# Performance work log

Hardware: AMD Instinct MI355X
Metric: run time of the kernel (lower is better)

Reference implementation:

```python
import jax, jax.numpy as jnp
import numpy as np

N = 100000   # nodes
E = 1600000  # edges
F = 128      # num_features
NF = 4       # n_factor
D = 64       # n_dim = dim // n_factor = 256 // 4
NL = 3       # n_layer
G = 128      # num graphs in batch


def setup_inputs() -> dict:
    key = jax.random.key(0)
    ks = jax.random.split(key, 10)
    s = 0.05
    x = jax.random.normal(ks[0], (N, F), jnp.float32)
    edge_index = jax.random.randint(ks[1], (2, E), 0, N)
    att = jax.random.uniform(ks[2], (NF, E), jnp.float32)
    batch = jnp.sort(jax.random.randint(ks[3], (N,), 0, G))
    lin_W = jax.random.normal(ks[4], (NF, F, D), jnp.float32) * s
    lin_b = jnp.zeros((NF, D), jnp.float32)
    conv_Wrel = jax.random.normal(ks[5], (NF, NL, D, D), jnp.float32) * s
    conv_brel = jnp.zeros((NF, NL, D), jnp.float32)
    conv_Wroot = jax.random.normal(ks[6], (NF, NL, D, D), jnp.float32) * s
    gru_Wih = jax.random.normal(ks[7], (NF, 3 * D, D), jnp.float32) * s
    gru_Whh = jax.random.normal(ks[8], (NF, 3 * D, D), jnp.float32) * s
    gru_bih = jnp.zeros((NF, 3 * D), jnp.float32)
    gru_bhh = jnp.zeros((NF, 3 * D), jnp.float32)
    return dict(x=x, edge_index=edge_index, att=att, batch=batch,
                lin_W=lin_W, lin_b=lin_b,
                conv_Wrel=conv_Wrel, conv_brel=conv_brel, conv_Wroot=conv_Wroot,
                gru_Wih=gru_Wih, gru_Whh=gru_Whh, gru_bih=gru_bih, gru_bhh=gru_bhh,
                num_graphs=G)


def _gru_cell(xin, h, Wih, Whh, bih, bhh):
    # torch.nn.GRU single step: r,z,n gates
    gi = xin @ Wih.T + bih  # [N, 3D]
    gh = h @ Whh.T + bhh
    ir, iz, inn = jnp.split(gi, 3, axis=-1)
    hr, hz, hn = jnp.split(gh, 3, axis=-1)
    r = jax.nn.sigmoid(ir + hr)
    z = jax.nn.sigmoid(iz + hz)
    n = jnp.tanh(inn + r * hn)
    return (1.0 - z) * n + z * h


def reference(x, edge_index, att, batch, lin_W, lin_b, conv_Wrel, conv_brel,
              conv_Wroot, gru_Wih, gru_Whh, gru_bih, gru_bhh, num_graphs):
    src, dst = edge_index[0], edge_index[1]
    counts = jax.ops.segment_sum(jnp.ones((N,), x.dtype), batch, num_segments=num_graphs)
    counts = jnp.maximum(counts, 1.0)[:, None]
    outs, feats = [], []
    for f in range(NF):
        w = att[f][:, None]                       # [E,1] edge weights for this factor
        out = x @ lin_W[f] + lin_b[f]             # [N,D]
        h = out                                   # initial GRU hidden state
        for l in range(NL):
            # GraphConv: lin_rel(scatter_add(w * x_src -> dst)) + lin_root(x)
            agg = jax.ops.segment_sum(out[src] * w, dst, num_segments=N)
            m = jax.nn.relu(agg @ conv_Wrel[f, l] + conv_brel[f, l] + out @ conv_Wroot[f, l])
            h = _gru_cell(m, h, gru_Wih[f], gru_Whh[f], gru_bih[f], gru_bhh[f])
            out = h
        feats.append(out)
        # global mean pool
        outs.append(jax.ops.segment_sum(out, batch, num_segments=num_graphs) / counts)
    return (jnp.stack(outs), jnp.stack(feats))
```

## Files before the change

kernel.cpp:

```cpp
#include <hip/hip_runtime.h>

#define NN   100000
#define EE   1600000
#define FDIM 128
#define NFAC 4
#define DD   64
#define NLAY 3
#define GG   128
#define ROW  (NFAC * DD)

#define PF_STRIDE 57344
#define OFF_WREL  8192
#define OFF_WROOT 20480
#define OFF_WIH   32768
#define OFF_WHH   45056
#define PREP_TOTAL (NFAC * PF_STRIDE)

typedef __bf16 bf16x8_t __attribute__((ext_vector_type(8)));
typedef float  f32x4_t  __attribute__((ext_vector_type(4)));

__device__ __forceinline__ unsigned short f2bf(float x) {
    unsigned u = __float_as_uint(x);
    u += 0x7fffu + ((u >> 16) & 1u);
    return (unsigned short)(u >> 16);
}
__device__ __forceinline__ float b2f(unsigned short h) {
    return __uint_as_float(((unsigned)h) << 16);
}
__device__ __forceinline__ float sigm(float x) { return 1.f / (1.f + __expf(-x)); }
__device__ __forceinline__ float tanh_f(float x) {
    float t = __expf(-2.f * fabsf(x));
    float r = (1.f - t) / (1.f + t);
    return x >= 0.f ? r : -r;
}

__global__ __launch_bounds__(256) void k_init(int* deg, int* cursor, float* outs) {
    int i = blockIdx.x * 256 + threadIdx.x;
    if (i < NN) { deg[i] = 0; cursor[i] = 0; }
    if (i < NFAC * GG * DD) outs[i] = 0.f;
}

__global__ __launch_bounds__(256) void k_prep(const float* x, const float* linW,
                                              const float* wrel, const float* wroot,
                                              const float* wih, const float* whh,
                                              unsigned short* x16, unsigned short* prep) {
    for (int i = blockIdx.x * 256 + threadIdx.x; i < NN * FDIM; i += gridDim.x * 256)
        x16[i] = f2bf(x[i]);
    for (int idx = blockIdx.x * 256 + threadIdx.x; idx < PREP_TOTAL; idx += gridDim.x * 256) {
        int f = idx / PF_STRIDE, r = idx % PF_STRIDE;
        int e, KB, mode, l = 0;
        if (r < OFF_WREL)       { e = r;                 KB = 4; mode = 0; }
        else if (r < OFF_WROOT) { int rr = r - OFF_WREL;  l = rr >> 12; e = rr & 4095; KB = 2; mode = 1; }
        else if (r < OFF_WIH)   { int rr = r - OFF_WROOT; l = rr >> 12; e = rr & 4095; KB = 2; mode = 2; }
        else if (r < OFF_WHH)   { e = r - OFF_WIH;        KB = 2; mode = 3; }
        else                    { e = r - OFF_WHH;        KB = 2; mode = 4; }
        int j = e & 7, lane = (e >> 3) & 63, t = e >> 9;
        int kb = t % KB, nt = t / KB;
        int k = kb * 32 + (lane >> 4) * 8 + j;
        int n = nt * 16 + (lane & 15);
        float v;
        if (mode == 0)      v = linW[(f * FDIM + k) * DD + n];
        else if (mode == 1) v = wrel[((f * 3 + l) * DD + k) * DD + n];
        else if (mode == 2) v = wroot[((f * 3 + l) * DD + k) * DD + n];
        else if (mode == 3) v = wih[(f * 192 + n) * DD + k];
        else                v = whh[(f * 192 + n) * DD + k];
        prep[idx] = f2bf(v);
    }
}

__global__ __launch_bounds__(256) void k_count(const int* batch, float* counts) {
    __shared__ int lb[GG + 1];
    int t = threadIdx.x;
    if (t <= GG) {
        int lo = 0, hi = NN;
        while (lo < hi) { int mid = (lo + hi) >> 1; if (batch[mid] < t) lo = mid + 1; else hi = mid; }
        lb[t] = lo;
    }
    __syncthreads();
    if (t < GG) counts[t] = (float)(lb[t + 1] - lb[t]);
}

__global__ __launch_bounds__(256) void k_deg(const int* ei, int* deg) {
    int e = blockIdx.x * 256 + threadIdx.x;
    if (e < EE) atomicAdd(&deg[ei[EE + e]], 1);
}
__global__ __launch_bounds__(256) void k_scan1(const int* deg, int* row_pos, int* bsum) {
    __shared__ int lds[256];
    int tid = threadIdx.x, idx = blockIdx.x * 256 + tid;
    int v = (idx < NN) ? deg[idx] : 0;
    lds[tid] = v; __syncthreads();
    for (int s = 1; s < 256; s <<= 1) {
        int t = (tid >= s) ? lds[tid - s] : 0;
        __syncthreads();
        lds[tid] += t;
        __syncthreads();
    }
    if (idx < NN) row_pos[idx] = lds[tid] - v;
    if (tid == 255) bsum[blockIdx.x] = lds[255];
}
__global__ __launch_bounds__(512) void k_scan2(int* bsum) {
    __shared__ int lds[512];
    int tid = threadIdx.x;
    int v = (tid < 391) ? bsum[tid] : 0;
    lds[tid] = v; __syncthreads();
    for (int s = 1; s < 512; s <<= 1) {
        int t = (tid >= s) ? lds[tid - s] : 0;
        __syncthreads();
        lds[tid] += t;
        __syncthreads();
    }
    bsum[tid] = lds[tid] - v;
}
__global__ __launch_bounds__(256) void k_rowptr(const int* row_pos, const int* boff, int* row_ptr) {
    int i = blockIdx.x * 256 + threadIdx.x;
    if (i < NN) row_ptr[i] = row_pos[i] + boff[i >> 8];
    if (i == 0) row_ptr[NN] = EE;
}
__global__ __launch_bounds__(256) void k_fill(const int* ei, const float* att,
                                              const int* row_ptr, int* cursor,
                                              int* csr_src, float* csr_att) {
    int e = blockIdx.x * 256 + threadIdx.x;
    if (e >= EE) return;
    int d = ei[EE + e];
    int slot = row_ptr[d] + atomicAdd(&cursor[d], 1);
    csr_src[slot] = ei[e];
    *(float4*)(csr_att + (size_t)slot * 4) =
        make_float4(att[e], att[EE + e], att[2 * EE + e], att[3 * EE + e]);
}

__global__ __launch_bounds__(256) void k_lin(const unsigned short* x16, const unsigned short* prep,
                                             const float* linb, unsigned short* out16) {
    int n0 = blockIdx.x * 64;
    __shared__ unsigned short xs[64 * 136];
    int tid = threadIdx.x;
    for (int t = tid; t < 1024; t += 256) {
        int row = t >> 4, seg = t & 15;
        int gn = n0 + row; if (gn >= NN) gn = NN - 1;
        *(uint4*)(xs + row * 136 + seg * 8) = *(const uint4*)(x16 + (size_t)gn * FDIM + seg * 8);
    }
    __syncthreads();
    int w = tid >> 6, lane = tid & 63, mrow = lane & 15, q = lane >> 4;
    const unsigned short* wp = prep + w * PF_STRIDE;
    bf16x8_t a[4][4];
#pragma unroll
    for (int mt = 0; mt < 4; mt++)
#pragma unroll
        for (int kb = 0; kb < 4; kb++)
            a[mt][kb] = *(const bf16x8_t*)(xs + (mt * 16 + mrow) * 136 + kb * 32 + q * 8);
#pragma unroll
    for (int nt = 0; nt < 4; nt++) {
        bf16x8_t b[4];
#pragma unroll
        for (int kb = 0; kb < 4; kb++)
            b[kb] = *(const bf16x8_t*)(wp + ((nt * 4 + kb) * 64 + lane) * 8);
        int col = nt * 16 + mrow;
        float bias = linb[w * DD + col];
#pragma unroll
        for (int mt = 0; mt < 4; mt++) {
            f32x4_t acc = {0.f, 0.f, 0.f, 0.f};
#pragma unroll
            for (int kb = 0; kb < 4; kb++)
                acc = __builtin_amdgcn_mfma_f32_16x16x32_bf16(a[mt][kb], b[kb], acc, 0, 0, 0);
#pragma unroll
            for (int r = 0; r < 4; r++) {
                int node = n0 + mt * 16 + q * 4 + r;
                if (node < NN) out16[(size_t)node * ROW + w * DD + col] = f2bf(acc[r] + bias);
            }
        }
    }
}

__global__ __launch_bounds__(256) void k_gather(const int* row_ptr, const int* csr_src, const float* csr_att,
                                                const unsigned short* out16, unsigned short* agg16) {
    int wave = threadIdx.x >> 6, lane = threadIdx.x & 63;
    int n = blockIdx.x * 4 + wave;
    if (n >= NN) return;
    int row = row_ptr[n], end = row_ptr[n + 1];
    int total = end - row;
    int fsel = lane >> 4, loff = lane * 4;
    float a0 = 0.f, a1 = 0.f, a2 = 0.f, a3 = 0.f;
    for (int base = 0; base < total; base += 8) {
        int s[8]; float w[8];
#pragma unroll
        for (int j = 0; j < 8; j++) {
            int e = base + j;
            int idx = row + (e < total ? e : total - 1);
            s[j] = csr_src[idx];
            float ww = csr_att[(size_t)idx * 4 + fsel];
            w[j] = (e < total) ? ww : 0.f;
        }
        uint2 v[8];
#pragma unroll
        for (int j = 0; j < 8; j++)
            v[j] = *(const uint2*)(out16 + (size_t)s[j] * ROW + loff);
#pragma unroll
        for (int j = 0; j < 8; j++) {
            a0 = fmaf(w[j], __uint_as_float(v[j].x << 16), a0);
            a1 = fmaf(w[j], __uint_as_float(v[j].x & 0xffff0000u), a1);
            a2 = fmaf(w[j], __uint_as_float(v[j].y << 16), a2);
            a3 = fmaf(w[j], __uint_as_float(v[j].y & 0xffff0000u), a3);
        }
    }
    ushort4 r;
    r.x = f2bf(a0); r.y = f2bf(a1); r.z = f2bf(a2); r.w = f2bf(a3);
    *(ushort4*)(agg16 + (size_t)n * ROW + loff) = r;
}

__global__ __launch_bounds__(256) void k_layer(int l, const unsigned short* agg16, unsigned short* out16,
                                               const unsigned short* prep, const float* brel,
                                               const float* bih, const float* bhh,
                                               float* feats, int last) {
    int f = blockIdx.y, n0 = blockIdx.x * 64;
    __shared__ unsigned short A1[64 * 72];
    __shared__ unsigned short A2[64 * 72];
    __shared__ unsigned short Mt[64 * 72];
    int tid = threadIdx.x;
    for (int t = tid; t < 512; t += 256) {
        int row = t >> 3, seg = t & 7;
        int gn = n0 + row; if (gn >= NN) gn = NN - 1;
        *(uint4*)(A1 + row * 72 + seg * 8) = *(const uint4*)(agg16 + (size_t)gn * ROW + f * DD + seg * 8);
        *(uint4*)(A2 + row * 72 + seg * 8) = *(const uint4*)(out16 + (size_t)gn * ROW + f * DD + seg * 8);
    }
    __syncthreads();
    int w = tid >> 6, lane = tid & 63, mrow = lane & 15, q = lane >> 4;
    const unsigned short* wrel  = prep + f * PF_STRIDE + OFF_WREL  + l * 4096;
    const unsigned short* wroot = prep + f * PF_STRIDE + OFF_WROOT + l * 4096;

    {
        bf16x8_t wr1[2], wr2[2];
#pragma unroll
        for (int kb = 0; kb < 2; kb++) {
            wr1[kb] = *(const bf16x8_t*)(wrel  + ((w * 2 + kb) * 64 + lane) * 8);
            wr2[kb] = *(const bf16x8_t*)(wroot + ((w * 2 + kb) * 64 + lane) * 8);
        }
        int col = w * 16 + mrow;
        float bias = brel[(f * 3 + l) * DD + col];
#pragma unroll
        for (int mt = 0; mt < 4; mt++) {
            f32x4_t acc = {0.f, 0.f, 0.f, 0.f};
#pragma unroll
            for (int kb = 0; kb < 2; kb++) {
                bf16x8_t a1 = *(const bf16x8_t*)(A1 + (mt * 16 + mrow) * 72 + kb * 32 + q * 8);
                acc = __builtin_amdgcn_mfma_f32_16x16x32_bf16(a1, wr1[kb], acc, 0, 0, 0);
                bf16x8_t a2 = *(const bf16x8_t*)(A2 + (mt * 16 + mrow) * 72 + kb * 32 + q * 8);
                acc = __builtin_amdgcn_mfma_f32_16x16x32_bf16(a2, wr2[kb], acc, 0, 0, 0);
            }
#pragma unroll
            for (int r = 0; r < 4; r++) {
                float mv = acc[r] + bias;
                mv = mv > 0.f ? mv : 0.f;
                Mt[(mt * 16 + q * 4 + r) * 72 + col] = f2bf(mv);
            }
        }
    }
    __syncthreads();

    const unsigned short* wih = prep + f * PF_STRIDE + OFF_WIH;
    const unsigned short* whh = prep + f * PF_STRIDE + OFF_WHH;
    bf16x8_t Br[2], Bz[2], Bn[2], Cr[2], Cz[2], Cn[2];
#pragma unroll
    for (int kb = 0; kb < 2; kb++) {
        Br[kb] = *(const bf16x8_t*)(wih + (((w)     * 2 + kb) * 64 + lane) * 8);
        Bz[kb] = *(const bf16x8_t*)(wih + (((w + 4) * 2 + kb) * 64 + lane) * 8);
        Bn[kb] = *(const bf16x8_t*)(wih + (((w + 8) * 2 + kb) * 64 + lane) * 8);
        Cr[kb] = *(const bf16x8_t*)(whh + (((w)     * 2 + kb) * 64 + lane) * 8);
        Cz[kb] = *(const bf16x8_t*)(whh + (((w + 4) * 2 + kb) * 64 + lane) * 8);
        Cn[kb] = *(const bf16x8_t*)(whh + (((w + 8) * 2 + kb) * 64 + lane) * 8);
    }
    int col = w * 16 + mrow;
    float bi_r = bih[f * 192 + col],        bh_r = bhh[f * 192 + col];
    float bi_z = bih[f * 192 + 64 + col],   bh_z = bhh[f * 192 + 64 + col];
    float bi_n = bih[f * 192 + 128 + col],  bh_n = bhh[f * 192 + 128 + col];
#pragma unroll
    for (int mt = 0; mt < 4; mt++) {
        f32x4_t ir = {0.f,0.f,0.f,0.f}, iz = {0.f,0.f,0.f,0.f}, in_ = {0.f,0.f,0.f,0.f};
        f32x4_t hr = {0.f,0.f,0.f,0.f}, hz = {0.f,0.f,0.f,0.f}, hn  = {0.f,0.f,0.f,0.f};
#pragma unroll
        for (int kb = 0; kb < 2; kb++) {
            bf16x8_t am = *(const bf16x8_t*)(Mt + (mt * 16 + mrow) * 72 + kb * 32 + q * 8);
            bf16x8_t ah = *(const bf16x8_t*)(A2 + (mt * 16 + mrow) * 72 + kb * 32 + q * 8);
            ir  = __builtin_amdgcn_mfma_f32_16x16x32_bf16(am, Br[kb], ir, 0, 0, 0);
            iz  = __builtin_amdgcn_mfma_f32_16x16x32_bf16(am, Bz[kb], iz, 0, 0, 0);
            in_ = __builtin_amdgcn_mfma_f32_16x16x32_bf16(am, Bn[kb], in_, 0, 0, 0);
            hr  = __builtin_amdgcn_mfma_f32_16x16x32_bf16(ah, Cr[kb], hr, 0, 0, 0);
            hz  = __builtin_amdgcn_mfma_f32_16x16x32_bf16(ah, Cz[kb], hz, 0, 0, 0);
            hn  = __builtin_amdgcn_mfma_f32_16x16x32_bf16(ah, Cn[kb], hn, 0, 0, 0);
        }
#pragma unroll
        for (int r = 0; r < 4; r++) {
            float rg = sigm(ir[r] + bi_r + hr[r] + bh_r);
            float z  = sigm(iz[r] + bi_z + hz[r] + bh_z);
            float nn = tanh_f(in_[r] + bi_n + rg * (hn[r] + bh_n));
            float h  = b2f(A2[(mt * 16 + q * 4 + r) * 72 + col]);
            float hp = (1.f - z) * nn + z * h;
            int node = n0 + mt * 16 + q * 4 + r;
            if (node < NN) {
                out16[(size_t)node * ROW + f * DD + col] = f2bf(hp);
                if (last) feats[((size_t)f * NN + node) * DD + col] = hp;
            }
        }
    }
}

__global__ __launch_bounds__(256) void k_pool(const float* feats, const int* batch, float* outs) {
    int f = blockIdx.y, w = threadIdx.x >> 6, lane = threadIdx.x & 63;
    int nbase = blockIdx.x * 256 + w * 64;
    if (nbase >= NN) return;
    int g_cur = batch[nbase];
    float acc = 0.f;
    for (int i = 0; i < 64; i++) {
        int n = nbase + i;
        if (n >= NN) break;
        int g = batch[n];
        float v = feats[((size_t)f * NN + n) * DD + lane];
        if (g != g_cur) {
            atomicAdd(&outs[(f * GG + g_cur) * DD + lane], acc);
            acc = v; g_cur = g;
        } else acc += v;
    }
    atomicAdd(&outs[(f * GG + g_cur) * DD + lane], acc);
}
__global__ __launch_bounds__(256) void k_norm(float* outs, const float* counts) {
    int i = blockIdx.x * 256 + threadIdx.x;
    if (i < NFAC * GG * DD) {
        int g = (i >> 6) & (GG - 1);
        outs[i] /= fmaxf(counts[g], 1.f);
    }
}

extern "C" void kernel_launch(void* const* d_in, const int* in_sizes, int n_in,
                              void* d_out, int out_size, void* d_ws, size_t ws_size,
                              hipStream_t stream) {
    const float* x    = (const float*)d_in[0];
    const int*   ei   = (const int*)d_in[1];
    const float* att  = (const float*)d_in[2];
    const int*   batch= (const int*)d_in[3];
    const float* linW = (const float*)d_in[4];
    const float* linb = (const float*)d_in[5];
    const float* wrel = (const float*)d_in[6];
    const float* brel = (const float*)d_in[7];
    const float* wroot= (const float*)d_in[8];
    const float* wih  = (const float*)d_in[9];
    const float* whh  = (const float*)d_in[10];
    const float* bih  = (const float*)d_in[11];
    const float* bhh  = (const float*)d_in[12];

    float* outs  = (float*)d_out;
    float* feats = (float*)d_out + NFAC * GG * DD;

    char* p = (char*)d_ws;
    unsigned short* out16 = (unsigned short*)p; p += (size_t)NN * ROW * 2;
    unsigned short* agg16 = (unsigned short*)p; p += (size_t)NN * ROW * 2;
    unsigned short* x16   = (unsigned short*)p; p += (size_t)NN * FDIM * 2;
    unsigned short* prep  = (unsigned short*)p; p += (size_t)PREP_TOTAL * 2;
    float* csr_att        = (float*)p;          p += (size_t)EE * 16;
    int* csr_src          = (int*)p;            p += (size_t)EE * 4;
    int* deg              = (int*)p;            p += (size_t)NN * 4;
    int* cursor           = (int*)p;            p += (size_t)NN * 4;
    int* row_pos          = (int*)p;            p += (size_t)NN * 4;
    int* row_ptr          = (int*)p;            p += (size_t)(NN + 1) * 4;
    int* boff             = (int*)p;            p += 512 * 4;
    float* counts         = (float*)p;          p += 512;

    k_init  <<<dim3(391),  dim3(256), 0, stream>>>(deg, cursor, outs);
    k_prep  <<<dim3(4096), dim3(256), 0, stream>>>(x, linW, wrel, wroot, wih, whh, x16, prep);
    k_count <<<dim3(1),    dim3(256), 0, stream>>>(batch, counts);
    k_deg   <<<dim3(6250), dim3(256), 0, stream>>>(ei, deg);
    k_scan1 <<<dim3(391),  dim3(256), 0, stream>>>(deg, row_pos, boff);
    k_scan2 <<<dim3(1),    dim3(512), 0, stream>>>(boff);
    k_rowptr<<<dim3(391),  dim3(256), 0, stream>>>(row_pos, boff, row_ptr);
    k_fill  <<<dim3(6250), dim3(256), 0, stream>>>(ei, att, row_ptr, cursor, csr_src, csr_att);
    k_lin   <<<dim3(1563), dim3(256), 0, stream>>>(x16, prep, linb, out16);
    for (int l = 0; l < NLAY; l++) {
        k_gather<<<dim3(25000),   dim3(256), 0, stream>>>(row_ptr, csr_src, csr_att, out16, agg16);
        k_layer <<<dim3(1563, 4), dim3(256), 0, stream>>>(l, agg16, out16, prep, brel, bih, bhh,
                                                          feats, (l == NLAY - 1) ? 1 : 0);
    }
    k_pool <<<dim3(391, 4), dim3(256), 0, stream>>>(feats, batch, outs);
    k_norm <<<dim3(128),    dim3(256), 0, stream>>>(outs, counts);
}
```

Baseline: 998.7 us.

## Switch node features to factor-major layout and split gather per factor

Node feature buffers change from node-major interleaved factors to factor-major [NF][N][D], and edge attention is stored as four per-factor arrays. The gather kernel now launches one grid slice per factor, with 16 lanes per node, so each factor's 12.8 MB feature table is gathered on its own and can stay resident in cache. The cost is that CSR source indices are read four times instead of once, and each gathered row becomes a 128-byte chunk rather than one 512-byte row.

```diff
diff --git a/kernel.cpp b/kernel.cpp
--- a/kernel.cpp
+++ b/kernel.cpp
@@ -7,7 +7,7 @@
 #define DD   64
 #define NLAY 3
 #define GG   128
-#define ROW  (NFAC * DD)
+
 
 #define PF_STRIDE 57344
 #define OFF_WREL  8192
@@ -118,14 +118,16 @@
 }
 __global__ __launch_bounds__(256) void k_fill(const int* ei, const float* att,
                                               const int* row_ptr, int* cursor,
-                                              int* csr_src, float* csr_att) {
+                                              int* csr_src, float* att_t) {
     int e = blockIdx.x * 256 + threadIdx.x;
     if (e >= EE) return;
     int d = ei[EE + e];
     int slot = row_ptr[d] + atomicAdd(&cursor[d], 1);
     csr_src[slot] = ei[e];
-    *(float4*)(csr_att + (size_t)slot * 4) =
-        make_float4(att[e], att[EE + e], att[2 * EE + e], att[3 * EE + e]);
+    att_t[slot]                  = att[e];
+    att_t[(size_t)EE + slot]     = att[EE + e];
+    att_t[(size_t)2 * EE + slot] = att[2 * EE + e];
+    att_t[(size_t)3 * EE + slot] = att[3 * EE + e];
 }
 
 __global__ __launch_bounds__(256) void k_lin(const unsigned short* x16, const unsigned short* prep,
@@ -164,20 +166,21 @@
 #pragma unroll
             for (int r = 0; r < 4; r++) {
                 int node = n0 + mt * 16 + q * 4 + r;
-                if (node < NN) out16[(size_t)node * ROW + w * DD + col] = f2bf(acc[r] + bias);
+                if (node < NN) out16[((size_t)w * NN + node) * DD + col] = f2bf(acc[r] + bias);
             }
         }
     }
 }
 
-__global__ __launch_bounds__(256) void k_gather(const int* row_ptr, const int* csr_src, const float* csr_att,
-                                                const unsigned short* out16, unsigned short* agg16) {
-    int wave = threadIdx.x >> 6, lane = threadIdx.x & 63;
-    int n = blockIdx.x * 4 + wave;
-    if (n >= NN) return;
+__global__ __launch_bounds__(256) void k_gather(const int* row_ptr, const int* csr_src, const float* att_t,
+                                                const unsigned short* in16, unsigned short* agg16) {
+    int tid = threadIdx.x, f = blockIdx.y;
+    int grp = tid >> 4, d4 = tid & 15;
+    int n = blockIdx.x * 16 + grp;
     int row = row_ptr[n], end = row_ptr[n + 1];
     int total = end - row;
-    int fsel = lane >> 4, loff = lane * 4;
+    const unsigned short* inf = in16 + (size_t)f * NN * DD;
+    const float* attf = att_t + (size_t)f * EE;
     float a0 = 0.f, a1 = 0.f, a2 = 0.f, a3 = 0.f;
     for (int base = 0; base < total; base += 8) {
         int s[8]; float w[8];
@@ -186,13 +189,13 @@
             int e = base + j;
             int idx = row + (e < total ? e : total - 1);
             s[j] = csr_src[idx];
-            float ww = csr_att[(size_t)idx * 4 + fsel];
+            float ww = attf[idx];
             w[j] = (e < total) ? ww : 0.f;
         }
         uint2 v[8];
 #pragma unroll
         for (int j = 0; j < 8; j++)
-            v[j] = *(const uint2*)(out16 + (size_t)s[j] * ROW + loff);
+            v[j] = *(const uint2*)(inf + (size_t)s[j] * DD + d4 * 4);
 #pragma unroll
         for (int j = 0; j < 8; j++) {
             a0 = fmaf(w[j], __uint_as_float(v[j].x << 16), a0);
@@ -203,7 +206,7 @@
     }
     ushort4 r;
     r.x = f2bf(a0); r.y = f2bf(a1); r.z = f2bf(a2); r.w = f2bf(a3);
-    *(ushort4*)(agg16 + (size_t)n * ROW + loff) = r;
+    *(ushort4*)(agg16 + ((size_t)f * NN + n) * DD + d4 * 4) = r;
 }
 
 __global__ __launch_bounds__(256) void k_layer(int l, const unsigned short* agg16, unsigned short* out16,
@@ -215,11 +218,13 @@
     __shared__ unsigned short A2[64 * 72];
     __shared__ unsigned short Mt[64 * 72];
     int tid = threadIdx.x;
+    const unsigned short* aggf = agg16 + (size_t)f * NN * DD;
+    const unsigned short* outf = out16 + (size_t)f * NN * DD;
     for (int t = tid; t < 512; t += 256) {
         int row = t >> 3, seg = t & 7;
         int gn = n0 + row; if (gn >= NN) gn = NN - 1;
-        *(uint4*)(A1 + row * 72 + seg * 8) = *(const uint4*)(agg16 + (size_t)gn * ROW + f * DD + seg * 8);
-        *(uint4*)(A2 + row * 72 + seg * 8) = *(const uint4*)(out16 + (size_t)gn * ROW + f * DD + seg * 8);
+        *(uint4*)(A1 + row * 72 + seg * 8) = *(const uint4*)(aggf + (size_t)gn * DD + seg * 8);
+        *(uint4*)(A2 + row * 72 + seg * 8) = *(const uint4*)(outf + (size_t)gn * DD + seg * 8);
     }
     __syncthreads();
     int w = tid >> 6, lane = tid & 63, mrow = lane & 15, q = lane >> 4;
@@ -271,6 +276,7 @@
     float bi_r = bih[f * 192 + col],        bh_r = bhh[f * 192 + col];
     float bi_z = bih[f * 192 + 64 + col],   bh_z = bhh[f * 192 + 64 + col];
     float bi_n = bih[f * 192 + 128 + col],  bh_n = bhh[f * 192 + 128 + col];
+    unsigned short* outwf = out16 + (size_t)f * NN * DD;
 #pragma unroll
     for (int mt = 0; mt < 4; mt++) {
         f32x4_t ir = {0.f,0.f,0.f,0.f}, iz = {0.f,0.f,0.f,0.f}, in_ = {0.f,0.f,0.f,0.f};
@@ -295,7 +301,7 @@
             float hp = (1.f - z) * nn + z * h;
             int node = n0 + mt * 16 + q * 4 + r;
             if (node < NN) {
-                out16[(size_t)node * ROW + f * DD + col] = f2bf(hp);
+                outwf[(size_t)node * DD + col] = f2bf(hp);
                 if (last) feats[((size_t)f * NN + node) * DD + col] = hp;
             }
         }
@@ -349,11 +355,11 @@
     float* feats = (float*)d_out + NFAC * GG * DD;
 
     char* p = (char*)d_ws;
-    unsigned short* out16 = (unsigned short*)p; p += (size_t)NN * ROW * 2;
-    unsigned short* agg16 = (unsigned short*)p; p += (size_t)NN * ROW * 2;
+    unsigned short* out16 = (unsigned short*)p; p += (size_t)NFAC * NN * DD * 2;
+    unsigned short* agg16 = (unsigned short*)p; p += (size_t)NFAC * NN * DD * 2;
     unsigned short* x16   = (unsigned short*)p; p += (size_t)NN * FDIM * 2;
     unsigned short* prep  = (unsigned short*)p; p += (size_t)PREP_TOTAL * 2;
-    float* csr_att        = (float*)p;          p += (size_t)EE * 16;
+    float* att_t          = (float*)p;          p += (size_t)EE * 16;
     int* csr_src          = (int*)p;            p += (size_t)EE * 4;
     int* deg              = (int*)p;            p += (size_t)NN * 4;
     int* cursor           = (int*)p;            p += (size_t)NN * 4;
@@ -369,10 +375,10 @@
     k_scan1 <<<dim3(391),  dim3(256), 0, stream>>>(deg, row_pos, boff);
     k_scan2 <<<dim3(1),    dim3(512), 0, stream>>>(boff);
     k_rowptr<<<dim3(391),  dim3(256), 0, stream>>>(row_pos, boff, row_ptr);
-    k_fill  <<<dim3(6250), dim3(256), 0, stream>>>(ei, att, row_ptr, cursor, csr_src, csr_att);
+    k_fill  <<<dim3(6250), dim3(256), 0, stream>>>(ei, att, row_ptr, cursor, csr_src, att_t);
     k_lin   <<<dim3(1563), dim3(256), 0, stream>>>(x16, prep, linb, out16);
     for (int l = 0; l < NLAY; l++) {
-        k_gather<<<dim3(25000),   dim3(256), 0, stream>>>(row_ptr, csr_src, csr_att, out16, agg16);
+        k_gather<<<dim3(6250, 4), dim3(256), 0, stream>>>(row_ptr, csr_src, att_t, out16, agg16);
         k_layer <<<dim3(1563, 4), dim3(256), 0, stream>>>(l, agg16, out16, prep, brel, bih, bhh,
                                                           feats, (l == NLAY - 1) ? 1 : 0);
     }
```

Result: slower. 1.085 ms (+8.6%).
